# Kernel optimization log

Measured on AMD Instinct MI355X. Metric: run time of the kernel, lower is better.

## Reference

```python
import jax, jax.numpy as jnp
import numpy as np

D_MODEL = 1024
NUM_HEADS = 16
HEAD_DIM = D_MODEL // NUM_HEADS
SCALE = HEAD_DIM ** -0.5
B, N = 4, 2048


def setup_inputs() -> dict:
    key = jax.random.key(0)
    ks = jax.random.split(key, 6)
    x = jax.random.normal(ks[0], (B, N, D_MODEL), dtype=jnp.float32)
    mask = jnp.ones((B, 1, N, N), dtype=jnp.int32)
    alibi_bias = jax.random.normal(ks[1], (1, NUM_HEADS, N, N), dtype=jnp.float32)
    s = 1.0 / np.sqrt(D_MODEL)
    Wq = jax.random.normal(ks[2], (D_MODEL, D_MODEL), dtype=jnp.float32) * s
    Wk = jax.random.normal(ks[3], (D_MODEL, D_MODEL), dtype=jnp.float32) * s
    Wv = jax.random.normal(ks[4], (D_MODEL, D_MODEL), dtype=jnp.float32) * s
    Wo = jax.random.normal(ks[5], (D_MODEL, D_MODEL), dtype=jnp.float32) * s
    return {"x": x, "mask": mask, "alibi_bias": alibi_bias,
            "Wq": Wq, "Wk": Wk, "Wv": Wv, "Wo": Wo}


def reference(x, mask, alibi_bias, Wq, Wk, Wv, Wo):
    Bx, Nx, D = x.shape
    H, Hd = NUM_HEADS, HEAD_DIM
    # torch Linear(bias=False): y = x @ W.T
    q = (x @ Wq.T).reshape(Bx, Nx, H, Hd).transpose(0, 2, 1, 3)  # [B,H,N,Hd]
    k = (x @ Wk.T).reshape(Bx, Nx, H, Hd).transpose(0, 2, 1, 3)
    v = (x @ Wv.T).reshape(Bx, Nx, H, Hd).transpose(0, 2, 1, 3)
    attn = jnp.einsum('bhqd,bhkd->bhqk', q, k) * SCALE
    attn = attn + alibi_bias
    neg_inf = jnp.finfo(attn.dtype).min
    attn = jnp.where(mask == 0, neg_inf, attn)
    attn = jax.nn.softmax(attn, axis=-1)
    out = jnp.einsum('bhqk,bhkd->bhqd', attn, v)  # [B,H,N,Hd]
    out = out.transpose(0, 2, 1, 3).reshape(Bx, Nx, D)
    return out @ Wo.T
```

## Files before the change

### kernel.cpp

```cpp
#include <hip/hip_runtime.h>

#define NSEQ 2048
#define DMODEL 1024
#define NHEAD 16
#define HDIM 64
#define NBATCH 4
#define MTOT 8192
#define ATT_SCALE 0.125f
#define LOG2E 1.4426950408889634f

typedef __bf16 bf16x8 __attribute__((ext_vector_type(8)));
typedef float f32x4 __attribute__((ext_vector_type(4)));
typedef unsigned int u32x4 __attribute__((ext_vector_type(4)));
typedef unsigned short u16;
typedef unsigned int u32;
typedef unsigned long long u64;

__device__ __forceinline__ u16 f2bf(float f) {
  u32 u = __builtin_bit_cast(u32, f);
  return (u16)((u + 0x7fffu + ((u >> 16) & 1u)) >> 16);
}

__device__ __forceinline__ void gload_lds16(const void* g, void* l) {
  __builtin_amdgcn_global_load_lds(
      (__attribute__((address_space(1))) const u32*)g,
      (__attribute__((address_space(3))) u32*)l, 16, 0, 0);
}

__global__ __launch_bounds__(256) void cast_f32_bf16(const float* __restrict__ in,
                                                     u16* __restrict__ out, int n) {
  int i = (blockIdx.x * 256 + threadIdx.x) * 4;
  if (i >= n) return;
  float4 v = *(const float4*)(in + i);
  ushort4 o;
  o.x = f2bf(v.x); o.y = f2bf(v.y); o.z = f2bf(v.z); o.w = f2bf(v.w);
  *(ushort4*)(out + i) = o;
}

__global__ __launch_bounds__(256) void cast_w4(const float* __restrict__ a,
                                               const float* __restrict__ b,
                                               const float* __restrict__ c,
                                               const float* __restrict__ d,
                                               u16* __restrict__ out) {
  int bid = blockIdx.x;
  int which = bid >> 10, lb = bid & 1023;
  const float* src = (which == 0) ? a : (which == 1) ? b : (which == 2) ? c : d;
  int i = (lb * 256 + threadIdx.x) * 4;
  float4 v = *(const float4*)(src + i);
  ushort4 o;
  o.x = f2bf(v.x); o.y = f2bf(v.y); o.z = f2bf(v.z); o.w = f2bf(v.w);
  *(ushort4*)(out + (size_t)which * 1048576 + i) = o;
}

__global__ __launch_bounds__(256) void pack_mask(const int* __restrict__ mask,
                                                 u64* __restrict__ bits) {
  int wave = (blockIdx.x * 256 + threadIdx.x) >> 6;
  int lane = threadIdx.x & 63;
  const int* row = mask + (size_t)wave * NSEQ;
  u64* out = bits + (size_t)wave * 32;
  for (int c = 0; c < 32; ++c) {
    int v = row[c * 64 + lane];
    u64 bl = __ballot(v != 0);
    if (lane == 0) out[c] = bl;
  }
}

__global__ __launch_bounds__(256) void gemm_qkv(const u16* __restrict__ A,
                                                const u16* __restrict__ Wc,
                                                u16* __restrict__ qo,
                                                u16* __restrict__ ko,
                                                u16* __restrict__ vo) {
  __shared__ __align__(16) u16 Al[128 * 64];
  __shared__ __align__(16) u16 Bl[128 * 64];
  const int tid = threadIdx.x;
  const int w = tid >> 6, l = tid & 63;
  const int l15 = l & 15, l4 = l >> 4;
  const int bm = blockIdx.x, bn = blockIdx.y;
  const int wm = w >> 1, wn = w & 1;

  f32x4 acc[4][4] = {};

  for (int ks = 0; ks < 1024; ks += 64) {
    __syncthreads();
#pragma unroll
    for (int c = 0; c < 4; ++c) {
      int g = w * 256 + c * 64 + l;
      int row = g >> 3, gc = g & 7;
      int sgc = gc ^ (row & 7);
      gload_lds16(A + (size_t)(bm * 128 + row) * 1024 + ks + sgc * 8, &Al[g * 8]);
      gload_lds16(Wc + (size_t)(bn * 128 + row) * 1024 + ks + sgc * 8, &Bl[g * 8]);
    }
    __syncthreads();
#pragma unroll
    for (int kc = 0; kc < 2; ++kc) {
      bf16x8 af[4], bfr[4];
#pragma unroll
      for (int mi = 0; mi < 4; ++mi) {
        int row = wm * 64 + mi * 16 + l15;
        int gc2 = (kc * 4 + l4) ^ (row & 7);
        af[mi] = *(const bf16x8*)&Al[row * 64 + gc2 * 8];
      }
#pragma unroll
      for (int ni = 0; ni < 4; ++ni) {
        int row = wn * 64 + ni * 16 + l15;
        int gc2 = (kc * 4 + l4) ^ (row & 7);
        bfr[ni] = *(const bf16x8*)&Bl[row * 64 + gc2 * 8];
      }
#pragma unroll
      for (int mi = 0; mi < 4; ++mi)
#pragma unroll
        for (int ni = 0; ni < 4; ++ni)
          acc[mi][ni] = __builtin_amdgcn_mfma_f32_16x16x32_bf16(af[mi], bfr[ni],
                                                                acc[mi][ni], 0, 0, 0);
    }
  }

  const int which = bn >> 3;
#pragma unroll
  for (int mi = 0; mi < 4; ++mi)
#pragma unroll
    for (int ni = 0; ni < 4; ++ni)
#pragma unroll
      for (int r = 0; r < 4; ++r) {
        int m = bm * 128 + wm * 64 + mi * 16 + l4 * 4 + r;
        int n = (bn & 7) * 128 + wn * 64 + ni * 16 + l15;
        int b = m >> 11, row = m & 2047, h = n >> 6, d = n & 63;
        u16 val = f2bf(acc[mi][ni][r]);
        size_t bh = (size_t)(b * 16 + h);
        if (which == 0)      qo[(bh * NSEQ + row) * 64 + d] = val;
        else if (which == 1) ko[(bh * NSEQ + row) * 64 + d] = val;
        else                 vo[(bh * 64 + d) * NSEQ + row] = val;
      }
}

__global__ __launch_bounds__(256) void gemm_out(const u16* __restrict__ A,
                                                const u16* __restrict__ W,
                                                float* __restrict__ C) {
  __shared__ __align__(16) u16 Al[128 * 64];
  __shared__ __align__(16) u16 Bl[128 * 64];
  const int tid = threadIdx.x;
  const int w = tid >> 6, l = tid & 63;
  const int l15 = l & 15, l4 = l >> 4;
  const int bm = blockIdx.x, bn = blockIdx.y;
  const int wm = w >> 1, wn = w & 1;

  f32x4 acc[4][4] = {};

  for (int ks = 0; ks < 1024; ks += 64) {
    __syncthreads();
#pragma unroll
    for (int c = 0; c < 4; ++c) {
      int g = w * 256 + c * 64 + l;
      int row = g >> 3, gc = g & 7;
      int sgc = gc ^ (row & 7);
      gload_lds16(A + (size_t)(bm * 128 + row) * 1024 + ks + sgc * 8, &Al[g * 8]);
      gload_lds16(W + (size_t)(bn * 128 + row) * 1024 + ks + sgc * 8, &Bl[g * 8]);
    }
    __syncthreads();
#pragma unroll
    for (int kc = 0; kc < 2; ++kc) {
      bf16x8 af[4], bfr[4];
#pragma unroll
      for (int mi = 0; mi < 4; ++mi) {
        int row = wm * 64 + mi * 16 + l15;
        int gc2 = (kc * 4 + l4) ^ (row & 7);
        af[mi] = *(const bf16x8*)&Al[row * 64 + gc2 * 8];
      }
#pragma unroll
      for (int ni = 0; ni < 4; ++ni) {
        int row = wn * 64 + ni * 16 + l15;
        int gc2 = (kc * 4 + l4) ^ (row & 7);
        bfr[ni] = *(const bf16x8*)&Bl[row * 64 + gc2 * 8];
      }
#pragma unroll
      for (int mi = 0; mi < 4; ++mi)
#pragma unroll
        for (int ni = 0; ni < 4; ++ni)
          acc[mi][ni] = __builtin_amdgcn_mfma_f32_16x16x32_bf16(af[mi], bfr[ni],
                                                                acc[mi][ni], 0, 0, 0);
    }
  }

#pragma unroll
  for (int mi = 0; mi < 4; ++mi)
#pragma unroll
    for (int ni = 0; ni < 4; ++ni)
#pragma unroll
      for (int r = 0; r < 4; ++r) {
        int m = bm * 128 + wm * 64 + mi * 16 + l4 * 4 + r;
        int n = bn * 128 + wn * 64 + ni * 16 + l15;
        C[(size_t)m * 1024 + n] = acc[mi][ni][r];
      }
}

__global__ __launch_bounds__(256, 4) void attn_kernel(
    const u16* __restrict__ q, const u16* __restrict__ k, const u16* __restrict__ vT,
    const float* __restrict__ alibi, const u64* __restrict__ mbits,
    u16* __restrict__ o) {
  __shared__ __align__(16) u16 Kl[2][64 * 64];
  __shared__ __align__(16) u16 Vl[2][64 * 64];

  const int tid = threadIdx.x, w = tid >> 6, l = tid & 63;
  const int l15 = l & 15, l4 = l >> 4;
  const int W = blockIdx.x;
  const int W2 = (W & 7) * 256 + (W >> 3);
  const int b = W2 & 3, hq = W2 >> 2;
  const int qb = hq & 31, h = hq >> 5;
  const int bh = b * 16 + h;
  const int wq0 = qb * 64 + w * 16;
  const int myq = wq0 + l15;

  bf16x8 aq[2];
  {
    const u16* qrow = q + ((size_t)bh * NSEQ + myq) * 64;
    aq[0] = *(const bf16x8*)(qrow + l4 * 8);
    aq[1] = *(const bf16x8*)(qrow + 32 + l4 * 8);
  }

  const u16* kg[2]; const u16* vg[2];
#pragma unroll
  for (int c = 0; c < 2; ++c) {
    int g = w * 128 + c * 64 + l;
    int row = g >> 3, gc = g & 7, sgc = gc ^ (row & 7);
    int srow = (row & 0x23) | (((row >> 2) & 3) << 3) | (((row >> 4) & 1) << 2);
    kg[c] = k + ((size_t)bh * NSEQ + srow) * 64 + sgc * 8;
    vg[c] = vT + ((size_t)bh * 64 + row) * NSEQ + sgc * 8;
  }

  const float* alp = alibi + (size_t)h * NSEQ * NSEQ + (size_t)myq * NSEQ + 8 * l4;
  const u64* mrp = mbits + ((size_t)b * NSEQ + myq) * 32;

  const int kfr[2] = { l15 * 128 + (((0 + l4) ^ (l15 & 7)) << 4),
                       l15 * 128 + (((4 + l4) ^ (l15 & 7)) << 4) };

  f32x4 oacc[4] = {};
  float m_run = -3.0e38f, l_run = 0.f;

  auto stage = [&](u16* KB, u16* VB) {
#pragma unroll
    for (int c = 0; c < 2; ++c) {
      gload_lds16(kg[c], (char*)KB + (w * 128 + c * 64 + l) * 16);
      kg[c] += 4096;
      gload_lds16(vg[c], (char*)VB + (w * 128 + c * 64 + l) * 16);
      vg[c] += 64;
    }
  };

  auto loadal = [&](float4* a, u64& m, int t) {
    a[0] = *(const float4*)(alp + t * 64);
    a[1] = *(const float4*)(alp + t * 64 + 4);
    a[2] = *(const float4*)(alp + t * 64 + 32);
    a[3] = *(const float4*)(alp + t * 64 + 36);
    m = mrp[t];
  };

  float4 alA[4], alB[4];
  u64 mbA, mbB;

  stage(Kl[0], Vl[0]);
  loadal(alA, mbA, 0);

  auto body = [&](const u16* KB, const u16* VB, u16* KN, u16* VN,
                  const float4* alc, u64 mbc, float4* aln, u64& mbn,
                  int t, bool dost) {
    if (dost) {
      loadal(aln, mbn, t + 1);
      asm volatile("s_waitcnt vmcnt(5)" ::: "memory");
    } else {
      asm volatile("s_waitcnt vmcnt(0)" ::: "memory");
    }
    __builtin_amdgcn_s_barrier();
    if (dost) stage(KN, VN);

    __builtin_amdgcn_s_setprio(1);
    f32x4 st[4];
#pragma unroll
    for (int kb = 0; kb < 4; ++kb) {
      f32x4 z = {0.f, 0.f, 0.f, 0.f};
      st[kb] = z;
#pragma unroll
      for (int kc = 0; kc < 2; ++kc) {
        bf16x8 bk = *(const bf16x8*)((const char*)KB + kfr[kc] + kb * 2048);
        st[kb] = __builtin_amdgcn_mfma_f32_16x16x32_bf16(bk, aq[kc], st[kb], 0, 0, 0);
      }
    }
    __builtin_amdgcn_s_setprio(0);

#pragma unroll
    for (int kb = 0; kb < 4; ++kb)
#pragma unroll
      for (int r = 0; r < 4; ++r)
        st[kb][r] = fmaf(st[kb][r], ATT_SCALE, alc[kb][r]);
    if (!__all(mbc == ~0ull)) {
#pragma unroll
      for (int kb = 0; kb < 4; ++kb)
#pragma unroll
        for (int r = 0; r < 4; ++r) {
          int bit = 32 * (kb >> 1) + 8 * l4 + 4 * (kb & 1) + r;
          if (!((mbc >> bit) & 1)) st[kb][r] = -3.0e38f;
        }
    }

    float m0 = fmaxf(fmaxf(st[0][0], st[0][1]), fmaxf(st[0][2], st[0][3]));
    float m1 = fmaxf(fmaxf(st[1][0], st[1][1]), fmaxf(st[1][2], st[1][3]));
    float m2 = fmaxf(fmaxf(st[2][0], st[2][1]), fmaxf(st[2][2], st[2][3]));
    float m3 = fmaxf(fmaxf(st[3][0], st[3][1]), fmaxf(st[3][2], st[3][3]));
    float tm = fmaxf(fmaxf(m0, m1), fmaxf(m2, m3));
    tm = fmaxf(tm, __shfl_xor(tm, 16));
    tm = fmaxf(tm, __shfl_xor(tm, 32));

    if (__any(tm > m_run + 4.0f)) {
      float mn = fmaxf(m_run, tm);
      float fac = exp2f((m_run - mn) * LOG2E);
      l_run *= fac;
      m_run = mn;
#pragma unroll
      for (int r = 0; r < 4; ++r) {
        float fr = __shfl(fac, l4 * 4 + r);
#pragma unroll
        for (int db = 0; db < 4; ++db) oacc[db][r] *= fr;
      }
    }

    float negm = -m_run * LOG2E;
    float p[16];
#pragma unroll
    for (int kb = 0; kb < 4; ++kb)
#pragma unroll
      for (int r = 0; r < 4; ++r)
        p[kb * 4 + r] = exp2f(fmaf(st[kb][r], LOG2E, negm));
    float s0 = (p[0] + p[1]) + (p[2] + p[3]);
    float s1 = (p[4] + p[5]) + (p[6] + p[7]);
    float s2 = (p[8] + p[9]) + (p[10] + p[11]);
    float s3 = (p[12] + p[13]) + (p[14] + p[15]);
    float ts = (s0 + s1) + (s2 + s3);
    ts += __shfl_xor(ts, 16);
    ts += __shfl_xor(ts, 32);
    l_run += ts;

    u32 Wp[8];
#pragma unroll
    for (int i = 0; i < 8; ++i)
      asm("v_cvt_pk_bf16_f32 %0, %1, %2" : "=v"(Wp[i]) : "v"(p[2 * i]), "v"(p[2 * i + 1]));

    __builtin_amdgcn_s_setprio(1);
#pragma unroll
    for (int c = 0; c < 2; ++c) {
      u32x4 wv = {Wp[4 * c], Wp[4 * c + 1], Wp[4 * c + 2], Wp[4 * c + 3]};
      bf16x8 pa = __builtin_bit_cast(bf16x8, wv);
#pragma unroll
      for (int db = 0; db < 4; ++db) {
        bf16x8 bv = *(const bf16x8*)((const char*)VB + kfr[c] + db * 2048);
        oacc[db] = __builtin_amdgcn_mfma_f32_16x16x32_bf16(pa, bv, oacc[db], 0, 0, 0);
      }
    }
    __builtin_amdgcn_s_setprio(0);
  };

  for (int t2 = 0; t2 < 16; ++t2) {
    body(Kl[0], Vl[0], Kl[1], Vl[1], alA, mbA, alB, mbB, t2 * 2, true);
    body(Kl[1], Vl[1], Kl[0], Vl[0], alB, mbB, alA, mbA, t2 * 2 + 1, t2 < 15);
  }

#pragma unroll
  for (int r = 0; r < 4; ++r) {
    float lr = __shfl(l_run, l4 * 4 + r);
    float inv = __builtin_amdgcn_rcpf(lr);
    int qq = wq0 + l4 * 4 + r;
#pragma unroll
    for (int db = 0; db < 4; ++db) {
      int d = db * 16 + l15;
      o[((size_t)b * NSEQ + qq) * DMODEL + h * 64 + d] = f2bf(oacc[db][r] * inv);
    }
  }
}

extern "C" void kernel_launch(void* const* d_in, const int* in_sizes, int n_in,
                              void* d_out, int out_size, void* d_ws, size_t ws_size,
                              hipStream_t stream) {
  (void)in_sizes; (void)n_in; (void)out_size; (void)ws_size;
  const float* x = (const float*)d_in[0];
  const int* mask = (const int*)d_in[1];
  const float* alibi = (const float*)d_in[2];
  const float* Wq = (const float*)d_in[3];
  const float* Wk = (const float*)d_in[4];
  const float* Wv = (const float*)d_in[5];
  const float* Wo = (const float*)d_in[6];
  float* out = (float*)d_out;

  char* ws = (char*)d_ws;
  const size_t MB = 1u << 20;
  u16* xb  = (u16*)(ws + 0 * MB);
  u16* wqb = (u16*)(ws + 16 * MB);
  u16* wob = (u16*)(ws + 22 * MB);
  u16* qb  = (u16*)(ws + 24 * MB);
  u16* kb  = (u16*)(ws + 40 * MB);
  u16* vT  = (u16*)(ws + 56 * MB);
  u16* ob  = (u16*)(ws + 72 * MB);
  u64* mbits = (u64*)(ws + 88 * MB);

  cast_f32_bf16<<<8192, 256, 0, stream>>>(x, xb, MTOT * DMODEL);
  cast_w4<<<4096, 256, 0, stream>>>(Wq, Wk, Wv, Wo, wqb);
  pack_mask<<<2048, 256, 0, stream>>>(mask, mbits);

  gemm_qkv<<<dim3(64, 24), 256, 0, stream>>>(xb, wqb, qb, kb, vT);

  attn_kernel<<<2048, 256, 0, stream>>>(qb, kb, vT, alibi, mbits, ob);

  gemm_out<<<dim3(64, 8), 256, 0, stream>>>(ob, wob, out);
}
```

Before: 397.9 us.

## Double attention block to 128 queries and simplify K/V staging sync

The attention kernel now launches 1024 blocks of 512 threads, each covering 128 queries instead of 64. This halves the number of times each K/V tile is staged into LDS per query, and each thread issues a single 16-byte load per buffer. The hand-tuned vmcnt waits, the mid-loop barrier and the setprio hints are replaced by one __syncthreads at the end of each iteration. That barrier likely drains the in-flight prefetch of the next tile, which weakens the overlap between loads and compute. The tighter launch bounds may also cap registers and cause spills.

```diff
diff --git a/kernel.cpp b/kernel.cpp
--- a/kernel.cpp
+++ b/kernel.cpp
@@ -193,7 +193,7 @@
       }
 }
 
-__global__ __launch_bounds__(256, 4) void attn_kernel(
+__global__ __launch_bounds__(512, 8) void attn_kernel(
     const u16* __restrict__ q, const u16* __restrict__ k, const u16* __restrict__ vT,
     const float* __restrict__ alibi, const u64* __restrict__ mbits,
     u16* __restrict__ o) {
@@ -203,11 +203,11 @@
   const int tid = threadIdx.x, w = tid >> 6, l = tid & 63;
   const int l15 = l & 15, l4 = l >> 4;
   const int W = blockIdx.x;
-  const int W2 = (W & 7) * 256 + (W >> 3);
+  const int W2 = (W & 7) * 128 + (W >> 3);
   const int b = W2 & 3, hq = W2 >> 2;
-  const int qb = hq & 31, h = hq >> 5;
+  const int qb = hq & 15, h = hq >> 4;
   const int bh = b * 16 + h;
-  const int wq0 = qb * 64 + w * 16;
+  const int wq0 = qb * 128 + w * 16;
   const int myq = wq0 + l15;
 
   bf16x8 aq[2];
@@ -217,14 +217,12 @@
     aq[1] = *(const bf16x8*)(qrow + 32 + l4 * 8);
   }
 
-  const u16* kg[2]; const u16* vg[2];
-#pragma unroll
-  for (int c = 0; c < 2; ++c) {
-    int g = w * 128 + c * 64 + l;
-    int row = g >> 3, gc = g & 7, sgc = gc ^ (row & 7);
+  const u16* kg; const u16* vg;
+  {
+    int row = tid >> 3, gc = tid & 7, sgc = gc ^ (row & 7);
     int srow = (row & 0x23) | (((row >> 2) & 3) << 3) | (((row >> 4) & 1) << 2);
-    kg[c] = k + ((size_t)bh * NSEQ + srow) * 64 + sgc * 8;
-    vg[c] = vT + ((size_t)bh * 64 + row) * NSEQ + sgc * 8;
+    kg = k + ((size_t)bh * NSEQ + srow) * 64 + sgc * 8;
+    vg = vT + ((size_t)bh * 64 + row) * NSEQ + sgc * 8;
   }
 
   const float* alp = alibi + (size_t)h * NSEQ * NSEQ + (size_t)myq * NSEQ + 8 * l4;
@@ -237,13 +235,10 @@
   float m_run = -3.0e38f, l_run = 0.f;
 
   auto stage = [&](u16* KB, u16* VB) {
-#pragma unroll
-    for (int c = 0; c < 2; ++c) {
-      gload_lds16(kg[c], (char*)KB + (w * 128 + c * 64 + l) * 16);
-      kg[c] += 4096;
-      gload_lds16(vg[c], (char*)VB + (w * 128 + c * 64 + l) * 16);
-      vg[c] += 64;
-    }
+    gload_lds16(kg, (char*)KB + tid * 16);
+    kg += 4096;
+    gload_lds16(vg, (char*)VB + tid * 16);
+    vg += 64;
   };
 
   auto loadal = [&](float4* a, u64& m, int t) {
@@ -259,20 +254,16 @@
 
   stage(Kl[0], Vl[0]);
   loadal(alA, mbA, 0);
+  __syncthreads();
 
   auto body = [&](const u16* KB, const u16* VB, u16* KN, u16* VN,
                   const float4* alc, u64 mbc, float4* aln, u64& mbn,
                   int t, bool dost) {
     if (dost) {
       loadal(aln, mbn, t + 1);
-      asm volatile("s_waitcnt vmcnt(5)" ::: "memory");
-    } else {
-      asm volatile("s_waitcnt vmcnt(0)" ::: "memory");
-    }
-    __builtin_amdgcn_s_barrier();
-    if (dost) stage(KN, VN);
-
-    __builtin_amdgcn_s_setprio(1);
+      stage(KN, VN);
+    }
+
     f32x4 st[4];
 #pragma unroll
     for (int kb = 0; kb < 4; ++kb) {
@@ -284,7 +275,6 @@
         st[kb] = __builtin_amdgcn_mfma_f32_16x16x32_bf16(bk, aq[kc], st[kb], 0, 0, 0);
       }
     }
-    __builtin_amdgcn_s_setprio(0);
 
 #pragma unroll
     for (int kb = 0; kb < 4; ++kb)
@@ -343,7 +333,6 @@
     for (int i = 0; i < 8; ++i)
       asm("v_cvt_pk_bf16_f32 %0, %1, %2" : "=v"(Wp[i]) : "v"(p[2 * i]), "v"(p[2 * i + 1]));
 
-    __builtin_amdgcn_s_setprio(1);
 #pragma unroll
     for (int c = 0; c < 2; ++c) {
       u32x4 wv = {Wp[4 * c], Wp[4 * c + 1], Wp[4 * c + 2], Wp[4 * c + 3]};
@@ -354,7 +343,7 @@
         oacc[db] = __builtin_amdgcn_mfma_f32_16x16x32_bf16(pa, bv, oacc[db], 0, 0, 0);
       }
     }
-    __builtin_amdgcn_s_setprio(0);
+    __syncthreads();
   };
 
   for (int t2 = 0; t2 < 16; ++t2) {
@@ -405,7 +394,7 @@
 
   gemm_qkv<<<dim3(64, 24), 256, 0, stream>>>(xb, wqb, qb, kb, vT);
 
-  attn_kernel<<<2048, 256, 0, stream>>>(qb, kb, vT, alibi, mbits, ob);
+  attn_kernel<<<1024, 512, 0, stream>>>(qb, kb, vT, alibi, mbits, ob);
 
   gemm_out<<<dim3(64, 8), 256, 0, stream>>>(ob, wob, out);
 }
```

After: 1.066 ms. +167.8%, slower.
